# Performance work log

Hardware: AMD Instinct MI355X
Metric: run time of the kernel (lower is better)

Reference implementation:

```python
import jax, jax.numpy as jnp
import numpy as np
from jax import lax

DIM = 512
IDIM = 1536
K = 7


def setup_inputs() -> dict:
    key = jax.random.key(0)
    ks = jax.random.split(key, 10)
    B, C, T = 16, DIM, 2048
    x = jax.random.normal(ks[0], (B, C, T), dtype=jnp.float32)
    dw_w = jax.random.normal(ks[1], (DIM, 1, K), dtype=jnp.float32) * (1.0 / np.sqrt(K))
    dw_b = jax.random.normal(ks[2], (DIM,), dtype=jnp.float32) * 0.01
    ln_g = jnp.ones((DIM,), dtype=jnp.float32)
    ln_b = jnp.zeros((DIM,), dtype=jnp.float32)
    w1 = jax.random.normal(ks[3], (IDIM, DIM), dtype=jnp.float32) * (1.0 / np.sqrt(DIM))
    b1 = jax.random.normal(ks[4], (IDIM,), dtype=jnp.float32) * 0.01
    grn_g = jax.random.normal(ks[5], (IDIM,), dtype=jnp.float32) * 0.02
    grn_b = jax.random.normal(ks[6], (IDIM,), dtype=jnp.float32) * 0.02
    w2 = jax.random.normal(ks[7], (DIM, IDIM), dtype=jnp.float32) * (1.0 / np.sqrt(IDIM))
    b2 = jax.random.normal(ks[8], (DIM,), dtype=jnp.float32) * 0.01
    return {"x": x, "dw_w": dw_w, "dw_b": dw_b, "ln_g": ln_g, "ln_b": ln_b,
            "w1": w1, "b1": b1, "grn_g": grn_g, "grn_b": grn_b, "w2": w2, "b2": b2}


def reference(x, dw_w, dw_b, ln_g, ln_b, w1, b1, grn_g, grn_b, w2, b2):
    residual = x  # [B, C, T]
    # depthwise conv1d, padding='same' style (K//2 each side)
    y = lax.conv_general_dilated(
        x, dw_w,
        window_strides=(1,),
        padding=[(K // 2, K // 2)],
        dimension_numbers=("NCH", "OIH", "NCH"),
        feature_group_count=DIM,
    ) + dw_b[None, :, None]
    y = jnp.transpose(y, (0, 2, 1))  # [B, T, C]
    # LayerNorm over channels, eps=1e-6
    mu = jnp.mean(y, axis=-1, keepdims=True)
    var = jnp.mean((y - mu) ** 2, axis=-1, keepdims=True)
    y = (y - mu) * lax.rsqrt(var + 1e-6) * ln_g + ln_b
    # pwconv1 + GELU (exact, erf-based as torch default)
    h = jnp.einsum("btc,ic->bti", y, w1) + b1  # [B, T, IDIM]
    h = jax.nn.gelu(h, approximate=False)
    # GRN: L2 norm over time axis (dim=1), mean over channels
    gx = jnp.sqrt(jnp.sum(h * h, axis=1, keepdims=True))  # [B, 1, IDIM]
    nx = gx / (jnp.mean(gx, axis=-1, keepdims=True) + 1e-6)
    h = grn_g * (h * nx) + grn_b + h
    # pwconv2
    y = jnp.einsum("bti,ci->btc", h, w2) + b2  # [B, T, C]
    y = jnp.transpose(y, (0, 2, 1))  # [B, C, T]
    return residual + y
```

## Files before the change

### kernel.cpp

```cpp
#include <hip/hip_runtime.h>
#include <math.h>

typedef unsigned short u16;
typedef unsigned int u32;
typedef __bf16 bf16x8_t __attribute__((ext_vector_type(8)));
typedef float f32x4_t __attribute__((ext_vector_type(4)));

__device__ __forceinline__ u16 f2bf(float f) {
  __bf16 b = (__bf16)f;
  return __builtin_bit_cast(u16, b);
}

__device__ __forceinline__ void gld16(const void* g, void* l) {
  __builtin_amdgcn_global_load_lds(
      (const __attribute__((address_space(1))) void*)g,
      (__attribute__((address_space(3))) void*)l, 16, 0, 0);
}

__device__ __forceinline__ float gelu_f(float v) {
  float z = 0.7978845608028654f * v * fmaf(0.044715f, v * v, 1.0f);
  float t = __builtin_amdgcn_exp2f(2.8853900817779268f * z);
  float r = __builtin_amdgcn_rcpf(t + 1.0f);
  return v - v * r;
}

__device__ __forceinline__ int swz8(int bid, int nwg) {
  int cpx = nwg >> 3;
  return (bid & 7) * cpx + (bid >> 3);
}

__global__ __launch_bounds__(256) void cast_kernel(const float* __restrict__ src,
                                                   u16* __restrict__ dst, int n) {
  int i = (blockIdx.x * 256 + threadIdx.x) * 4;
  if (i < n) {
    float4 v = *(const float4*)(src + i);
    uint2 o;
    o.x = (u32)f2bf(v.x) | ((u32)f2bf(v.y) << 16);
    o.y = (u32)f2bf(v.z) | ((u32)f2bf(v.w) << 16);
    *(uint2*)(dst + i) = o;
  }
}

__global__ __launch_bounds__(64) void b2ob_kernel(const float* __restrict__ w2,
                                                  const float* __restrict__ grn_b,
                                                  const float* __restrict__ b2,
                                                  float* __restrict__ out) {
  int c = blockIdx.x;
  int l = threadIdx.x;
  float p = 0.f;
  for (int i = l; i < 1536; i += 64) p += grn_b[i] * w2[(size_t)c * 1536 + i];
  #pragma unroll
  for (int s = 32; s; s >>= 1) p += __shfl_xor(p, s);
  if (l == 0) out[c] = b2[c] + p;
}

__global__ __launch_bounds__(512, 4) void conv_ln_kernel(const float* __restrict__ X,
                                                         const float* __restrict__ Wd,
                                                         const float* __restrict__ bd,
                                                         const float* __restrict__ lng,
                                                         const float* __restrict__ lnb,
                                                         u16* __restrict__ Y) {
  __shared__ float ystage[16 * 516];
  __shared__ float mu_s[16], rs_s[16];

  const int c = threadIdx.x;
  const int b = blockIdx.y;
  const int t0 = blockIdx.x * 64;

  const float* xr = X + ((size_t)b * 512 + c) * 2048;
  float wr[7];
  #pragma unroll
  for (int k = 0; k < 7; ++k) wr[k] = Wd[c * 7 + k];
  const float bdv = bd[c];
  const float lg = lng[c];
  const float lb = lnb[c];

  for (int ch = 0; ch < 4; ++ch) {
    const int tc0 = t0 + ch * 16;
    const int g = tc0 - 4;
    float w[24];
    if (g >= 0 && g + 24 <= 2048) {
      #pragma unroll
      for (int q = 0; q < 6; ++q) {
        float4 v = *(const float4*)(xr + g + q * 4);
        w[q * 4 + 0] = v.x; w[q * 4 + 1] = v.y;
        w[q * 4 + 2] = v.z; w[q * 4 + 3] = v.w;
      }
    } else {
      #pragma unroll
      for (int j = 0; j < 24; ++j) {
        int tt = g + j;
        w[j] = (tt >= 0 && tt < 2048) ? xr[tt] : 0.f;
      }
    }
    float outv[16];
    #pragma unroll
    for (int i = 0; i < 16; ++i) {
      float a = bdv;
      #pragma unroll
      for (int k = 0; k < 7; ++k) a = fmaf(w[i + 1 + k], wr[k], a);
      outv[i] = a;
      ystage[i * 516 + c] = a;
    }
    __syncthreads();
    {
      int r = c >> 5, cl = c & 31;
      float s = 0.f, q = 0.f;
      #pragma unroll
      for (int k = 0; k < 16; ++k) {
        float v = ystage[r * 516 + cl + k * 32];
        s += v; q += v * v;
      }
      #pragma unroll
      for (int m = 16; m; m >>= 1) { s += __shfl_xor(s, m); q += __shfl_xor(q, m); }
      if (cl == 0) {
        float mu = s * (1.f / 512.f);
        float var = q * (1.f / 512.f) - mu * mu;
        mu_s[r] = mu;
        rs_s[r] = rsqrtf(var + 1e-6f);
      }
    }
    __syncthreads();
    #pragma unroll
    for (int i = 0; i < 16; ++i) {
      float v = (outv[i] - mu_s[i]) * rs_s[i] * lg + lb;
      Y[(size_t)(b * 2048 + tc0 + i) * 512 + c] = f2bf(v);
    }
  }
}

__global__ __launch_bounds__(256) void grn_kernel(const float* __restrict__ gsum,
                                                  const float* __restrict__ grn_g,
                                                  float* __restrict__ svec) {
  __shared__ float red[256];
  int b = blockIdx.x, tid = threadIdx.x;
  float gx[6];
  float part = 0.f;
  #pragma unroll
  for (int it = 0; it < 6; ++it) {
    int i = it * 256 + tid;
    gx[it] = sqrtf(gsum[b * 1536 + i]);
    part += gx[it];
  }
  red[tid] = part;
  __syncthreads();
  for (int s = 128; s; s >>= 1) {
    if (tid < s) red[tid] += red[tid + s];
    __syncthreads();
  }
  float inv = 1.0f / (red[0] * (1.f / 1536.f) + 1e-6f);
  #pragma unroll
  for (int it = 0; it < 6; ++it) {
    int i = it * 256 + tid;
    svec[b * 1536 + i] = 1.0f + grn_g[i] * gx[it] * inv;
  }
}

__global__ __launch_bounds__(256) void w2s_kernel(const float* __restrict__ w2,
                                                  const float* __restrict__ svec,
                                                  u16* __restrict__ out) {
  size_t e0 = ((size_t)blockIdx.x * 256 + threadIdx.x) * 8;
  int i = (int)(e0 % 1536);
  size_t bc = e0 / 1536;
  int b = (int)(bc >> 9);
  size_t widx = (bc & 511) * 1536 + i;
  float4 wa = *(const float4*)(w2 + widx);
  float4 wb = *(const float4*)(w2 + widx + 4);
  float4 sa = *(const float4*)(svec + b * 1536 + i);
  float4 sb = *(const float4*)(svec + b * 1536 + i + 4);
  uint4 o;
  o.x = (u32)f2bf(wa.x * sa.x) | ((u32)f2bf(wa.y * sa.y) << 16);
  o.y = (u32)f2bf(wa.z * sa.z) | ((u32)f2bf(wa.w * sa.w) << 16);
  o.z = (u32)f2bf(wb.x * sb.x) | ((u32)f2bf(wb.y * sb.y) << 16);
  o.w = (u32)f2bf(wb.z * sb.z) | ((u32)f2bf(wb.w * sb.w) << 16);
  *(uint4*)(out + e0) = o;
}

template<int KD>
__device__ __forceinline__ void gemm_kloop(const u16* __restrict__ Ag,
                                           const u16* __restrict__ Bg,
                                           u16* lds, int NT,
                                           f32x4_t (&acc)[4][4]) {
  const int tid = threadIdx.x;
  const int l = tid & 63, l15 = l & 15, lq = l >> 4;
  const int w = tid >> 6;
  const int wm = w >> 1, wn = w & 1;
  const int rin = tid >> 3;
  const int cs = ((tid & 7) ^ (rin & 7)) << 3;

  auto STAGE = [&](int buf, int kt) {
    u16* lA = lds + buf * 16384;
    u16* lB = lA + 8192;
    #pragma unroll
    for (int c = 0; c < 4; ++c) {
      gld16(Ag + (size_t)(c * 32 + rin) * KD + kt + cs, lA + (c * 32 + w * 8) * 64);
      gld16(Bg + (size_t)(c * 32 + rin) * KD + kt + cs, lB + (c * 32 + w * 8) * 64);
    }
  };

  STAGE(0, 0);
  __syncthreads();

  for (int S = 0; S < NT; ++S) {
    const int cur = S & 1;
    if (S + 1 < NT) STAGE(cur ^ 1, (S + 1) * 64);
    u16* lA = lds + cur * 16384;
    u16* lB = lA + 8192;
    bf16x8_t af[4][2], bf[4][2];
    #pragma unroll
    for (int f = 0; f < 4; ++f) {
      const int Ra = wm * 64 + f * 16 + l15;
      const int Rb = wn * 64 + f * 16 + l15;
      #pragma unroll
      for (int kk = 0; kk < 2; ++kk) {
        af[f][kk] = *(const bf16x8_t*)(lA + Ra * 64 + (((kk * 4 + lq) ^ (Ra & 7)) << 3));
        bf[f][kk] = *(const bf16x8_t*)(lB + Rb * 64 + (((kk * 4 + lq) ^ (Rb & 7)) << 3));
      }
    }
    #pragma unroll
    for (int i = 0; i < 4; ++i)
      #pragma unroll
      for (int j = 0; j < 4; ++j)
        #pragma unroll
        for (int kk = 0; kk < 2; ++kk)
          acc[i][j] = __builtin_amdgcn_mfma_f32_16x16x32_bf16(af[i][kk], bf[j][kk], acc[i][j], 0, 0, 0);
    __syncthreads();
  }
}

__global__ __launch_bounds__(256) void gemm1_kernel(const u16* __restrict__ A,
                                                    const u16* __restrict__ Bw,
                                                    const float* __restrict__ b1,
                                                    u16* __restrict__ H,
                                                    float* __restrict__ gsum) {
  extern __shared__ __align__(16) u16 lds[];
  const int tid = threadIdx.x;
  const int l = tid & 63, l15 = l & 15, lq = l >> 4;
  const int w = tid >> 6, wm = w >> 1, wn = w & 1;
  const int wg = swz8(blockIdx.x, 3072);
  const int ntile = wg % 12, mtile = wg / 12;
  const int m0 = mtile * 128, n0 = ntile * 128;
  const int bidx = m0 >> 11;

  f32x4_t acc[4][4];
  #pragma unroll
  for (int i = 0; i < 4; ++i)
    #pragma unroll
    for (int j = 0; j < 4; ++j) {
      f32x4_t z = {0.f, 0.f, 0.f, 0.f};
      acc[i][j] = z;
    }

  gemm_kloop<512>(A + (size_t)m0 * 512, Bw + (size_t)n0 * 512, lds, 8, acc);

  float bj[4];
  #pragma unroll
  for (int nf = 0; nf < 4; ++nf) bj[nf] = b1[n0 + wn * 64 + nf * 16 + l15];

  float ss[4] = {0.f, 0.f, 0.f, 0.f};
  #pragma unroll
  for (int mf = 0; mf < 4; ++mf) {
    const int lr = wm * 64 + mf * 16 + lq * 4;
    #pragma unroll
    for (int nf = 0; nf < 4; ++nf) {
      const int cl = wn * 64 + nf * 16 + l15;
      #pragma unroll
      for (int r = 0; r < 4; ++r) {
        float g = gelu_f(acc[mf][nf][r] + bj[nf]);
        ss[nf] += g * g;
        lds[(lr + r) * 130 + cl] = f2bf(g);
      }
    }
  }
  #pragma unroll
  for (int nf = 0; nf < 4; ++nf) {
    float v = ss[nf];
    v += __shfl_xor(v, 16);
    v += __shfl_xor(v, 32);
    if (lq == 0) atomicAdd(&gsum[bidx * 1536 + n0 + wn * 64 + nf * 16 + l15], v);
  }
  __syncthreads();
  #pragma unroll
  for (int it = 0; it < 8; ++it) {
    int idx = it * 256 + tid;
    int row = idx >> 4, ch = idx & 15;
    uint4 v = *(const uint4*)(lds + row * 130 + ch * 8);
    *(uint4*)(H + (size_t)(m0 + row) * 1536 + n0 + ch * 8) = v;
  }
}

__global__ __launch_bounds__(256) void gemm2_kernel(const u16* __restrict__ Hm,
                                                    const u16* __restrict__ W2s,
                                                    const float* __restrict__ b2ob,
                                                    const float* __restrict__ X,
                                                    float* __restrict__ Out) {
  extern __shared__ __align__(16) u16 lds[];
  const int tid = threadIdx.x;
  const int l = tid & 63, l15 = l & 15, lq = l >> 4;
  const int w = tid >> 6, wm = w >> 1, wn = w & 1;
  const int wg = swz8(blockIdx.x, 1024);
  const int ntile = wg & 3, mtile = wg >> 2;
  const int m0 = mtile * 128, n0 = ntile * 128;
  const int bidx = m0 >> 11, t0 = m0 & 2047;

  f32x4_t acc[4][4];
  #pragma unroll
  for (int i = 0; i < 4; ++i)
    #pragma unroll
    for (int j = 0; j < 4; ++j) {
      f32x4_t z = {0.f, 0.f, 0.f, 0.f};
      acc[i][j] = z;
    }

  gemm_kloop<1536>(Hm + (size_t)m0 * 1536,
                   W2s + ((size_t)bidx * 512 + n0) * 1536, lds, 24, acc);

  float* st = (float*)lds;
  for (int half = 0; half < 2; ++half) {
    __syncthreads();
    if (wm == half) {
      #pragma unroll
      for (int mf = 0; mf < 4; ++mf) {
        const int lr = mf * 16 + lq * 4;
        #pragma unroll
        for (int nf = 0; nf < 4; ++nf) {
          const int cl = wn * 64 + nf * 16 + l15;
          #pragma unroll
          for (int r = 0; r < 4; ++r)
            st[(lr + r) * 129 + cl] = acc[mf][nf][r];
        }
      }
    }
    __syncthreads();
    const size_t obase = ((size_t)bidx * 512 + n0) * 2048 + (size_t)(t0 + half * 64 + l);
    #pragma unroll
    for (int cc = 0; cc < 32; ++cc) {
      const int c = w * 32 + cc;
      float v = st[l * 129 + c] + b2ob[n0 + c];
      size_t oi = obase + (size_t)c * 2048;
      Out[oi] = v + X[oi];
    }
  }
}

extern "C" void kernel_launch(void* const* d_in, const int* in_sizes, int n_in,
                              void* d_out, int out_size, void* d_ws, size_t ws_size,
                              hipStream_t stream) {
  const float* x     = (const float*)d_in[0];
  const float* dw_w  = (const float*)d_in[1];
  const float* dw_b  = (const float*)d_in[2];
  const float* ln_g  = (const float*)d_in[3];
  const float* ln_b  = (const float*)d_in[4];
  const float* w1    = (const float*)d_in[5];
  const float* b1    = (const float*)d_in[6];
  const float* grn_g = (const float*)d_in[7];
  const float* grn_b = (const float*)d_in[8];
  const float* w2    = (const float*)d_in[9];
  const float* b2    = (const float*)d_in[10];
  float* out = (float*)d_out;

  u16* y_ln = (u16*)d_ws;
  u16* w2s  = y_ln;
  u16* h    = y_ln + (size_t)32768 * 512;
  u16* w1b  = h + (size_t)32768 * 1536;
  float* gsum = (float*)(w1b + (size_t)1536 * 512);
  float* svec = gsum + 16 * 1536;
  float* b2ob = svec + 16 * 1536;

  (void)hipFuncSetAttribute((const void*)gemm1_kernel,
                            hipFuncAttributeMaxDynamicSharedMemorySize, 65536);
  (void)hipFuncSetAttribute((const void*)gemm2_kernel,
                            hipFuncAttributeMaxDynamicSharedMemorySize, 65536);

  hipMemsetAsync(gsum, 0, 16 * 1536 * sizeof(float), stream);
  cast_kernel<<<768, 256, 0, stream>>>(w1, w1b, 1536 * 512);
  b2ob_kernel<<<512, 64, 0, stream>>>(w2, grn_b, b2, b2ob);
  conv_ln_kernel<<<dim3(32, 16), 512, 0, stream>>>(x, dw_w, dw_b, ln_g, ln_b, y_ln);
  gemm1_kernel<<<3072, 256, 65536, stream>>>(y_ln, w1b, b1, h, gsum);
  grn_kernel<<<16, 256, 0, stream>>>(gsum, grn_g, svec);
  w2s_kernel<<<6144, 256, 0, stream>>>(w2, svec, w2s);
  gemm2_kernel<<<1024, 256, 65536, stream>>>(h, w2s, b2ob, x, out);
}
```

Baseline: 227.3 us.

## Enlarge GEMM tiles to 256x256 with 8 waves per workgroup

Both GEMM kernels move from 128x128 tiles with 4 waves to 256x256 tiles with 512 threads. Each wave now computes a 128x64 sub-tile with an 8x4 accumulator array, and B fragments are loaded once and reused across 8 A fragments. The aim is to raise arithmetic intensity and cut global and LDS traffic per MFMA. In exchange, LDS use doubles to 128KB per block, which limits each CU to one block. Accumulator register pressure also grows, and gemm2's grid shrinks to 256 blocks, giving a single wave with little latency hiding. The epilogues are split into halves and quarters so they fit in LDS.

After: 274.2 us. 1.21x slower.

```diff
diff --git a/kernel.cpp b/kernel.cpp
--- a/kernel.cpp
+++ b/kernel.cpp
@@ -180,22 +180,24 @@
 __device__ __forceinline__ void gemm_kloop(const u16* __restrict__ Ag,
                                            const u16* __restrict__ Bg,
                                            u16* lds, int NT,
-                                           f32x4_t (&acc)[4][4]) {
+                                           f32x4_t (&acc)[8][4]) {
   const int tid = threadIdx.x;
   const int l = tid & 63, l15 = l & 15, lq = l >> 4;
   const int w = tid >> 6;
-  const int wm = w >> 1, wn = w & 1;
+  const int wm = w >> 2, wn = w & 3;
   const int rin = tid >> 3;
   const int cs = ((tid & 7) ^ (rin & 7)) << 3;
+  const int wb = w * 512;
 
   auto STAGE = [&](int buf, int kt) {
-    u16* lA = lds + buf * 16384;
-    u16* lB = lA + 8192;
-    #pragma unroll
-    for (int c = 0; c < 4; ++c) {
-      gld16(Ag + (size_t)(c * 32 + rin) * KD + kt + cs, lA + (c * 32 + w * 8) * 64);
-      gld16(Bg + (size_t)(c * 32 + rin) * KD + kt + cs, lB + (c * 32 + w * 8) * 64);
-    }
+    u16* lA = lds + buf * 32768;
+    u16* lB = lA + 16384;
+    #pragma unroll
+    for (int c = 0; c < 4; ++c)
+      gld16(Ag + (size_t)(c * 64 + rin) * KD + kt + cs, lA + c * 4096 + wb);
+    #pragma unroll
+    for (int c = 0; c < 4; ++c)
+      gld16(Bg + (size_t)(c * 64 + rin) * KD + kt + cs, lB + c * 4096 + wb);
   };
 
   STAGE(0, 0);
@@ -204,47 +206,48 @@
   for (int S = 0; S < NT; ++S) {
     const int cur = S & 1;
     if (S + 1 < NT) STAGE(cur ^ 1, (S + 1) * 64);
-    u16* lA = lds + cur * 16384;
-    u16* lB = lA + 8192;
-    bf16x8_t af[4][2], bf[4][2];
-    #pragma unroll
-    for (int f = 0; f < 4; ++f) {
-      const int Ra = wm * 64 + f * 16 + l15;
-      const int Rb = wn * 64 + f * 16 + l15;
-      #pragma unroll
-      for (int kk = 0; kk < 2; ++kk) {
-        af[f][kk] = *(const bf16x8_t*)(lA + Ra * 64 + (((kk * 4 + lq) ^ (Ra & 7)) << 3));
-        bf[f][kk] = *(const bf16x8_t*)(lB + Rb * 64 + (((kk * 4 + lq) ^ (Rb & 7)) << 3));
-      }
-    }
-    #pragma unroll
-    for (int i = 0; i < 4; ++i)
-      #pragma unroll
-      for (int j = 0; j < 4; ++j)
-        #pragma unroll
-        for (int kk = 0; kk < 2; ++kk)
-          acc[i][j] = __builtin_amdgcn_mfma_f32_16x16x32_bf16(af[i][kk], bf[j][kk], acc[i][j], 0, 0, 0);
-    __syncthreads();
-  }
-}
-
-__global__ __launch_bounds__(256) void gemm1_kernel(const u16* __restrict__ A,
-                                                    const u16* __restrict__ Bw,
-                                                    const float* __restrict__ b1,
-                                                    u16* __restrict__ H,
-                                                    float* __restrict__ gsum) {
+    u16* lA = lds + cur * 32768;
+    u16* lB = lA + 16384;
+    bf16x8_t bfr[4][2];
+    #pragma unroll
+    for (int g = 0; g < 4; ++g) {
+      const int Rb = wn * 64 + g * 16 + l15;
+      #pragma unroll
+      for (int kk = 0; kk < 2; ++kk)
+        bfr[g][kk] = *(const bf16x8_t*)(lB + Rb * 64 + (((kk * 4 + lq) ^ (Rb & 7)) << 3));
+    }
+    #pragma unroll
+    for (int i = 0; i < 8; ++i) {
+      const int Ra = wm * 128 + i * 16 + l15;
+      bf16x8_t a0 = *(const bf16x8_t*)(lA + Ra * 64 + ((lq ^ (Ra & 7)) << 3));
+      bf16x8_t a1 = *(const bf16x8_t*)(lA + Ra * 64 + (((4 + lq) ^ (Ra & 7)) << 3));
+      #pragma unroll
+      for (int j = 0; j < 4; ++j) {
+        acc[i][j] = __builtin_amdgcn_mfma_f32_16x16x32_bf16(a0, bfr[j][0], acc[i][j], 0, 0, 0);
+        acc[i][j] = __builtin_amdgcn_mfma_f32_16x16x32_bf16(a1, bfr[j][1], acc[i][j], 0, 0, 0);
+      }
+    }
+    __syncthreads();
+  }
+}
+
+__global__ __launch_bounds__(512, 2) void gemm1_kernel(const u16* __restrict__ A,
+                                                       const u16* __restrict__ Bw,
+                                                       const float* __restrict__ b1,
+                                                       u16* __restrict__ H,
+                                                       float* __restrict__ gsum) {
   extern __shared__ __align__(16) u16 lds[];
   const int tid = threadIdx.x;
   const int l = tid & 63, l15 = l & 15, lq = l >> 4;
-  const int w = tid >> 6, wm = w >> 1, wn = w & 1;
-  const int wg = swz8(blockIdx.x, 3072);
-  const int ntile = wg % 12, mtile = wg / 12;
-  const int m0 = mtile * 128, n0 = ntile * 128;
+  const int w = tid >> 6, wm = w >> 2, wn = w & 3;
+  const int wg = swz8(blockIdx.x, 768);
+  const int ntile = wg % 6, mtile = wg / 6;
+  const int m0 = mtile * 256, n0 = ntile * 256;
   const int bidx = m0 >> 11;
 
-  f32x4_t acc[4][4];
-  #pragma unroll
-  for (int i = 0; i < 4; ++i)
+  f32x4_t acc[8][4];
+  #pragma unroll
+  for (int i = 0; i < 8; ++i)
     #pragma unroll
     for (int j = 0; j < 4; ++j) {
       f32x4_t z = {0.f, 0.f, 0.f, 0.f};
@@ -253,23 +256,36 @@
 
   gemm_kloop<512>(A + (size_t)m0 * 512, Bw + (size_t)n0 * 512, lds, 8, acc);
 
+  const int coll = wn * 64 + l15;
   float bj[4];
   #pragma unroll
-  for (int nf = 0; nf < 4; ++nf) bj[nf] = b1[n0 + wn * 64 + nf * 16 + l15];
+  for (int nf = 0; nf < 4; ++nf) bj[nf] = b1[n0 + coll + nf * 16];
 
   float ss[4] = {0.f, 0.f, 0.f, 0.f};
-  #pragma unroll
-  for (int mf = 0; mf < 4; ++mf) {
-    const int lr = wm * 64 + mf * 16 + lq * 4;
-    #pragma unroll
-    for (int nf = 0; nf < 4; ++nf) {
-      const int cl = wn * 64 + nf * 16 + l15;
-      #pragma unroll
-      for (int r = 0; r < 4; ++r) {
-        float g = gelu_f(acc[mf][nf][r] + bj[nf]);
-        ss[nf] += g * g;
-        lds[(lr + r) * 130 + cl] = f2bf(g);
-      }
+  for (int half = 0; half < 2; ++half) {
+    __syncthreads();
+    if (wm == half) {
+      #pragma unroll
+      for (int mf = 0; mf < 8; ++mf) {
+        const int lr = mf * 16 + lq * 4;
+        #pragma unroll
+        for (int nf = 0; nf < 4; ++nf) {
+          #pragma unroll
+          for (int r = 0; r < 4; ++r) {
+            float g = gelu_f(acc[mf][nf][r] + bj[nf]);
+            ss[nf] += g * g;
+            lds[(lr + r) * 264 + coll + nf * 16] = f2bf(g);
+          }
+        }
+      }
+    }
+    __syncthreads();
+    #pragma unroll
+    for (int it = 0; it < 8; ++it) {
+      int idx = it * 512 + tid;
+      int row = idx >> 5, ch = idx & 31;
+      uint4 v = *(const uint4*)(lds + row * 264 + ch * 8);
+      *(uint4*)(H + (size_t)(m0 + half * 128 + row) * 1536 + n0 + ch * 8) = v;
     }
   }
   #pragma unroll
@@ -277,35 +293,27 @@
     float v = ss[nf];
     v += __shfl_xor(v, 16);
     v += __shfl_xor(v, 32);
-    if (lq == 0) atomicAdd(&gsum[bidx * 1536 + n0 + wn * 64 + nf * 16 + l15], v);
-  }
-  __syncthreads();
-  #pragma unroll
-  for (int it = 0; it < 8; ++it) {
-    int idx = it * 256 + tid;
-    int row = idx >> 4, ch = idx & 15;
-    uint4 v = *(const uint4*)(lds + row * 130 + ch * 8);
-    *(uint4*)(H + (size_t)(m0 + row) * 1536 + n0 + ch * 8) = v;
-  }
-}
-
-__global__ __launch_bounds__(256) void gemm2_kernel(const u16* __restrict__ Hm,
-                                                    const u16* __restrict__ W2s,
-                                                    const float* __restrict__ b2ob,
-                                                    const float* __restrict__ X,
-                                                    float* __restrict__ Out) {
+    if (lq == 0) atomicAdd(&gsum[bidx * 1536 + n0 + coll + nf * 16], v);
+  }
+}
+
+__global__ __launch_bounds__(512, 2) void gemm2_kernel(const u16* __restrict__ Hm,
+                                                       const u16* __restrict__ W2s,
+                                                       const float* __restrict__ b2ob,
+                                                       const float* __restrict__ X,
+                                                       float* __restrict__ Out) {
   extern __shared__ __align__(16) u16 lds[];
   const int tid = threadIdx.x;
   const int l = tid & 63, l15 = l & 15, lq = l >> 4;
-  const int w = tid >> 6, wm = w >> 1, wn = w & 1;
-  const int wg = swz8(blockIdx.x, 1024);
-  const int ntile = wg & 3, mtile = wg >> 2;
-  const int m0 = mtile * 128, n0 = ntile * 128;
+  const int w = tid >> 6, wm = w >> 2, wn = w & 3;
+  const int wg = swz8(blockIdx.x, 256);
+  const int ntile = wg & 1, mtile = wg >> 1;
+  const int m0 = mtile * 256, n0 = ntile * 256;
   const int bidx = m0 >> 11, t0 = m0 & 2047;
 
-  f32x4_t acc[4][4];
-  #pragma unroll
-  for (int i = 0; i < 4; ++i)
+  f32x4_t acc[8][4];
+  #pragma unroll
+  for (int i = 0; i < 8; ++i)
     #pragma unroll
     for (int j = 0; j < 4; ++j) {
       f32x4_t z = {0.f, 0.f, 0.f, 0.f};
@@ -316,27 +324,28 @@
                    W2s + ((size_t)bidx * 512 + n0) * 1536, lds, 24, acc);
 
   float* st = (float*)lds;
-  for (int half = 0; half < 2; ++half) {
-    __syncthreads();
-    if (wm == half) {
-      #pragma unroll
-      for (int mf = 0; mf < 4; ++mf) {
-        const int lr = mf * 16 + lq * 4;
+  for (int grp = 0; grp < 4; ++grp) {
+    __syncthreads();
+    if (wm == (grp >> 1)) {
+      #pragma unroll
+      for (int m2 = 0; m2 < 4; ++m2) {
+        const int mf = (grp & 1) * 4 + m2;
+        const int lr = m2 * 16 + lq * 4;
         #pragma unroll
         for (int nf = 0; nf < 4; ++nf) {
           const int cl = wn * 64 + nf * 16 + l15;
           #pragma unroll
           for (int r = 0; r < 4; ++r)
-            st[(lr + r) * 129 + cl] = acc[mf][nf][r];
+            st[(lr + r) * 261 + cl] = acc[mf][nf][r];
         }
       }
     }
     __syncthreads();
-    const size_t obase = ((size_t)bidx * 512 + n0) * 2048 + (size_t)(t0 + half * 64 + l);
+    const size_t obase = ((size_t)bidx * 512 + n0) * 2048 + (size_t)(t0 + grp * 64 + l);
     #pragma unroll
     for (int cc = 0; cc < 32; ++cc) {
       const int c = w * 32 + cc;
-      float v = st[l * 129 + c] + b2ob[n0 + c];
+      float v = st[l * 261 + c] + b2ob[n0 + c];
       size_t oi = obase + (size_t)c * 2048;
       Out[oi] = v + X[oi];
     }
@@ -368,16 +377,16 @@
   float* b2ob = svec + 16 * 1536;
 
   (void)hipFuncSetAttribute((const void*)gemm1_kernel,
-                            hipFuncAttributeMaxDynamicSharedMemorySize, 65536);
+                            hipFuncAttributeMaxDynamicSharedMemorySize, 131072);
   (void)hipFuncSetAttribute((const void*)gemm2_kernel,
-                            hipFuncAttributeMaxDynamicSharedMemorySize, 65536);
+                            hipFuncAttributeMaxDynamicSharedMemorySize, 131072);
 
   hipMemsetAsync(gsum, 0, 16 * 1536 * sizeof(float), stream);
   cast_kernel<<<768, 256, 0, stream>>>(w1, w1b, 1536 * 512);
   b2ob_kernel<<<512, 64, 0, stream>>>(w2, grn_b, b2, b2ob);
   conv_ln_kernel<<<dim3(32, 16), 512, 0, stream>>>(x, dw_w, dw_b, ln_g, ln_b, y_ln);
-  gemm1_kernel<<<3072, 256, 65536, stream>>>(y_ln, w1b, b1, h, gsum);
+  gemm1_kernel<<<768, 512, 131072, stream>>>(y_ln, w1b, b1, h, gsum);
   grn_kernel<<<16, 256, 0, stream>>>(gsum, grn_g, svec);
   w2s_kernel<<<6144, 256, 0, stream>>>(w2, svec, w2s);
-  gemm2_kernel<<<1024, 256, 65536, stream>>>(h, w2s, b2ob, x, out);
-}
+  gemm2_kernel<<<256, 512, 131072, stream>>>(h, w2s, b2ob, x, out);
+}
```
